# Performance work log

Hardware: AMD Instinct MI355X
Metric: run time of the kernel (lower is better)

Reference implementation:

```python
import jax, jax.numpy as jnp
import numpy as np

N_C, N_S, D = 16384, 16384, 2688  # 128x128 hypercolumn grid, VGG16 concat channels
EPS = 1e-8


def setup_inputs() -> dict:
    key = jax.random.key(0)
    k1, k2 = jax.random.split(key)
    feats_c = jax.random.normal(k1, (N_C, D), dtype=jnp.float32)
    feats_s = jax.random.normal(k2, (N_S, D), dtype=jnp.float32)
    return {"feats_c": feats_c, "feats_s": feats_s}


def reference(feats_c, feats_s):
    # NNST replace_features: for each content hypercolumn vector, find the
    # style feature vector with max cosine similarity and take it as target.
    cn = feats_c * jax.lax.rsqrt(jnp.sum(feats_c * feats_c, axis=1, keepdims=True) + EPS)
    sn = feats_s * jax.lax.rsqrt(jnp.sum(feats_s * feats_s, axis=1, keepdims=True) + EPS)
    sim = jnp.einsum("cd,sd->cs", cn, sn)  # [N_C, N_S] cosine similarity
    idx = jnp.argmax(sim, axis=1)           # nearest style feature per content pixel
    target_feats = jnp.take(feats_s, idx, axis=0)  # gather un-normalized style feats
    return target_feats
```

## Files before the change

### kernel.cpp

```cpp
#include <hip/hip_runtime.h>
#include <stdint.h>

typedef unsigned short ushort_t;
typedef unsigned int u32;
typedef unsigned long long u64;

#define NC_ 16384
#define NS_ 16384
#define DIM 2688
#define D4 (DIM / 4)
#define KSTEPS (DIM / 32)

typedef __attribute__((ext_vector_type(8))) short short8;
typedef __attribute__((ext_vector_type(4))) float f32x4;


__device__ inline ushort_t f2bf(float x) {
  u32 u = __float_as_uint(x);
  u32 r = u + 0x7FFFu + ((u >> 16) & 1u);
  return (ushort_t)(r >> 16);
}
__device__ inline float bf2f(ushort_t b) { return __uint_as_float(((u32)b) << 16); }

__device__ inline u32 fkey(float f) {
  u32 u = __float_as_uint(f);
  return (u & 0x80000000u) ? ~u : (u | 0x80000000u);
}

__device__ inline void async16(const void* g, void* l) {
  __builtin_amdgcn_global_load_lds(
      (const __attribute__((address_space(1))) u32*)g,
      (__attribute__((address_space(3))) u32*)l, 16, 0, 0);
}


__global__ __launch_bounds__(256) void content_split_kernel(
    const float* __restrict__ fc, ushort_t* __restrict__ c_hi, ushort_t* __restrict__ c_lo) {
  size_t i = (size_t)blockIdx.x * 256 + threadIdx.x;
  if (i >= (size_t)NC_ * DIM / 4) return;
  float4 v = ((const float4*)fc)[i];
  ushort4 h, l;
  h.x = f2bf(v.x); l.x = f2bf(v.x - bf2f(h.x));
  h.y = f2bf(v.y); l.y = f2bf(v.y - bf2f(h.y));
  h.z = f2bf(v.z); l.z = f2bf(v.z - bf2f(h.z));
  h.w = f2bf(v.w); l.w = f2bf(v.w - bf2f(h.w));
  ((ushort4*)c_hi)[i] = h;
  ((ushort4*)c_lo)[i] = l;
}


__global__ __launch_bounds__(256) void style_split_kernel(
    const float* __restrict__ fs, ushort_t* __restrict__ s_hi, ushort_t* __restrict__ s_lo) {
  const int s = blockIdx.x, t = threadIdx.x;
  const float4* row = (const float4*)(fs + (size_t)s * DIM);
  float ss = 0.f;
  for (int i = t; i < D4; i += 256) {
    float4 v = row[i];
    ss += v.x * v.x + v.y * v.y + v.z * v.z + v.w * v.w;
  }
#pragma unroll
  for (int off = 32; off >= 1; off >>= 1) ss += __shfl_xor(ss, off, 64);
  __shared__ float wsum[4];
  if ((t & 63) == 0) wsum[t >> 6] = ss;
  __syncthreads();
  float scale = rsqrtf(wsum[0] + wsum[1] + wsum[2] + wsum[3] + 1e-8f);
  ushort4* h4 = (ushort4*)(s_hi + (size_t)s * DIM);
  ushort4* l4 = (ushort4*)(s_lo + (size_t)s * DIM);
  for (int i = t; i < D4; i += 256) {
    float4 v = row[i];
    float x = v.x * scale, y = v.y * scale, z = v.z * scale, w = v.w * scale;
    ushort4 h, l;
    h.x = f2bf(x); l.x = f2bf(x - bf2f(h.x));
    h.y = f2bf(y); l.y = f2bf(y - bf2f(h.y));
    h.z = f2bf(z); l.z = f2bf(z - bf2f(h.z));
    h.w = f2bf(w); l.w = f2bf(w - bf2f(h.w));
    h4[i] = h;
    l4[i] = l;
  }
}


__global__ __launch_bounds__(256) void sim_argmax_kernel(
    const ushort_t* __restrict__ c_hi, const ushort_t* __restrict__ c_lo,
    const ushort_t* __restrict__ s_hi, const ushort_t* __restrict__ s_lo,
    u64* __restrict__ partial) {
  __shared__ __align__(16) ushort_t lds[4 * 128 * 32];
  __shared__ u64 red[256];

  ushort_t* la_hi = lds;
  ushort_t* la_lo = lds + 4096;
  ushort_t* lb_hi = lds + 8192;
  ushort_t* lb_lo = lds + 12288;

  const int t = threadIdx.x;
  const int bid = blockIdx.x;
  const int grp = bid >> 8;
  const int wi = bid & 255;
  const int cb = (grp & 7) * 16 + (wi & 15);
  const int sb = (grp >> 3) * 16 + (wi >> 4);

  const ushort_t* gah = c_hi + (size_t)cb * 128 * DIM;
  const ushort_t* gal = c_lo + (size_t)cb * 128 * DIM;
  const ushort_t* gbh = s_hi + (size_t)sb * 128 * DIM;
  const ushort_t* gbl = s_lo + (size_t)sb * 128 * DIM;

  const int lane = t & 63;
  const int wave = t >> 6;
  const int wy = wave >> 1, wx = wave & 1;
  const int lm = lane & 15, q = lane >> 4;

  f32x4 acc[4][4];
#pragma unroll
  for (int i = 0; i < 4; i++)
#pragma unroll
    for (int j = 0; j < 4; j++) acc[i][j] = (f32x4){0.f, 0.f, 0.f, 0.f};

  const int tw = t & 192;

  for (int ks = 0; ks < KSTEPS; ++ks) {
    const int kel = ks * 32;
#pragma unroll
    for (int j = 0; j < 2; ++j) {
      int e = j * 256 + t;
      int row = e >> 2, c4 = e & 3;
      size_t goff = (size_t)row * DIM + kel + c4 * 8;
      int loff = (j * 256 + tw) * 8;
      async16(gah + goff, la_hi + loff);
      async16(gal + goff, la_lo + loff);
      async16(gbh + goff, lb_hi + loff);
      async16(gbl + goff, lb_lo + loff);
    }
    __syncthreads();

    short8 ah[4], al[4], bh[4], bl[4];
#pragma unroll
    for (int mi = 0; mi < 4; ++mi) {
      int r = (wy * 64 + mi * 16 + lm) * 32 + q * 8;
      ah[mi] = *(const short8*)(la_hi + r);
      al[mi] = *(const short8*)(la_lo + r);
    }
#pragma unroll
    for (int ni = 0; ni < 4; ++ni) {
      int r = (wx * 64 + ni * 16 + lm) * 32 + q * 8;
      bh[ni] = *(const short8*)(lb_hi + r);
      bl[ni] = *(const short8*)(lb_lo + r);
    }
#pragma unroll
    for (int mi = 0; mi < 4; ++mi)
#pragma unroll
      for (int ni = 0; ni < 4; ++ni) {
        acc[mi][ni] = __builtin_amdgcn_mfma_f32_16x16x32_bf16(ah[mi], bh[ni], acc[mi][ni], 0, 0, 0);
        acc[mi][ni] = __builtin_amdgcn_mfma_f32_16x16x32_bf16(ah[mi], bl[ni], acc[mi][ni], 0, 0, 0);
        acc[mi][ni] = __builtin_amdgcn_mfma_f32_16x16x32_bf16(al[mi], bh[ni], acc[mi][ni], 0, 0, 0);
      }
    __syncthreads();
  }

#pragma unroll
  for (int mi = 0; mi < 4; ++mi) {
#pragma unroll
    for (int r = 0; r < 4; ++r) {
      float bv = acc[mi][0][r];
      int bn = 0;
#pragma unroll
      for (int ni = 1; ni < 4; ++ni) {
        float v = acc[mi][ni][r];
        if (v > bv) { bv = v; bn = ni; }
      }
      u32 colg = (u32)(sb * 128 + wx * 64 + bn * 16 + lm);
      u64 key = ((u64)fkey(bv) << 32) | (u64)(0xFFFFFFFFu - colg);
#pragma unroll
      for (int off = 8; off >= 1; off >>= 1) {
        u64 o = __shfl_xor((unsigned long long)key, off, 64);
        if (o > key) key = o;
      }
      if (lm == 0) red[(wy * 64 + mi * 16 + q * 4 + r) * 2 + wx] = key;
    }
  }
  __syncthreads();
  if (t < 128) {
    u64 k0 = red[t * 2], k1 = red[t * 2 + 1];
    u64 b = k0 > k1 ? k0 : k1;
    partial[((size_t)(cb * 128 + t)) * 128 + sb] = b;
  }
}


__global__ __launch_bounds__(256) void argmax_gather_kernel(
    const u64* __restrict__ partial, const float* __restrict__ fs, float* __restrict__ out) {
  const int m = blockIdx.x, t = threadIdx.x;
  __shared__ u64 sred[2];
  u64 key = 0;
  if (t < 128) key = partial[(size_t)m * 128 + t];
#pragma unroll
  for (int off = 32; off >= 1; off >>= 1) {
    u64 o = __shfl_xor((unsigned long long)key, off, 64);
    if (o > key) key = o;
  }
  if (t < 128 && (t & 63) == 0) sred[t >> 6] = key;
  __syncthreads();
  u64 best = sred[0] > sred[1] ? sred[0] : sred[1];
  u32 col = 0xFFFFFFFFu - (u32)best;
  const float4* src = (const float4*)(fs + (size_t)col * DIM);
  float4* dst = (float4*)(out + (size_t)m * DIM);
  for (int i = t; i < D4; i += 256) dst[i] = src[i];
}


extern "C" void kernel_launch(void* const* d_in, const int* in_sizes, int n_in,
                              void* d_out, int out_size, void* d_ws, size_t ws_size,
                              hipStream_t stream) {
  const float* fc = (const float*)d_in[0];
  const float* fs = (const float*)d_in[1];
  float* out = (float*)d_out;

  ushort_t* c_hi = (ushort_t*)d_ws;
  ushort_t* c_lo = c_hi + (size_t)NC_ * DIM;
  ushort_t* s_hi = c_lo + (size_t)NC_ * DIM;
  ushort_t* s_lo = s_hi + (size_t)NS_ * DIM;
  u64* partial = (u64*)(s_lo + (size_t)NS_ * DIM);

  content_split_kernel<<<(NC_ * DIM / 4 + 255) / 256, 256, 0, stream>>>(fc, c_hi, c_lo);
  style_split_kernel<<<NS_, 256, 0, stream>>>(fs, s_hi, s_lo);
  sim_argmax_kernel<<<16384, 256, 0, stream>>>(c_hi, c_lo, s_hi, s_lo, partial);
  argmax_gather_kernel<<<NC_, 256, 0, stream>>>(partial, fs, out);
}
```

Baseline: 4.686 ms.

## Widen similarity tile to 128x256 and XOR-swizzle LDS layout

```diff
diff --git a/kernel.cpp b/kernel.cpp
--- a/kernel.cpp
+++ b/kernel.cpp
@@ -31,6 +31,10 @@
   __builtin_amdgcn_global_load_lds(
       (const __attribute__((address_space(1))) u32*)g,
       (__attribute__((address_space(3))) u32*)l, 16, 0, 0);
+}
+
+__device__ inline int swz(int r, int q) {
+  return ((r >> 1) << 6) + (((((r & 1) << 2) | q) ^ ((r >> 1) & 7)) << 3);
 }
 
 
@@ -80,17 +84,17 @@
 }
 
 
-__global__ __launch_bounds__(256) void sim_argmax_kernel(
+__global__ __launch_bounds__(256, 2) void sim_argmax_kernel(
     const ushort_t* __restrict__ c_hi, const ushort_t* __restrict__ c_lo,
     const ushort_t* __restrict__ s_hi, const ushort_t* __restrict__ s_lo,
     u64* __restrict__ partial) {
-  __shared__ __align__(16) ushort_t lds[4 * 128 * 32];
-  __shared__ u64 red[256];
+  __shared__ __align__(16) ushort_t lds[24576];
+  __shared__ u64 red[128][2];
 
   ushort_t* la_hi = lds;
   ushort_t* la_lo = lds + 4096;
   ushort_t* lb_hi = lds + 8192;
-  ushort_t* lb_lo = lds + 12288;
+  ushort_t* lb_lo = lds + 16384;
 
   const int t = threadIdx.x;
   const int bid = blockIdx.x;
@@ -101,19 +105,19 @@
 
   const ushort_t* gah = c_hi + (size_t)cb * 128 * DIM;
   const ushort_t* gal = c_lo + (size_t)cb * 128 * DIM;
-  const ushort_t* gbh = s_hi + (size_t)sb * 128 * DIM;
-  const ushort_t* gbl = s_lo + (size_t)sb * 128 * DIM;
+  const ushort_t* gbh = s_hi + (size_t)sb * 256 * DIM;
+  const ushort_t* gbl = s_lo + (size_t)sb * 256 * DIM;
 
   const int lane = t & 63;
   const int wave = t >> 6;
   const int wy = wave >> 1, wx = wave & 1;
   const int lm = lane & 15, q = lane >> 4;
 
-  f32x4 acc[4][4];
+  f32x4 acc[4][8];
 #pragma unroll
   for (int i = 0; i < 4; i++)
 #pragma unroll
-    for (int j = 0; j < 4; j++) acc[i][j] = (f32x4){0.f, 0.f, 0.f, 0.f};
+    for (int j = 0; j < 8; j++) acc[i][j] = (f32x4){0.f, 0.f, 0.f, 0.f};
 
   const int tw = t & 192;
 
@@ -122,37 +126,53 @@
 #pragma unroll
     for (int j = 0; j < 2; ++j) {
       int e = j * 256 + t;
-      int row = e >> 2, c4 = e & 3;
-      size_t goff = (size_t)row * DIM + kel + c4 * 8;
+      int rp = e >> 3;
+      int cc = (e & 7) ^ (rp & 7);
+      int row = (rp << 1) | (cc >> 2);
+      size_t goff = (size_t)row * DIM + kel + (cc & 3) * 8;
       int loff = (j * 256 + tw) * 8;
       async16(gah + goff, la_hi + loff);
       async16(gal + goff, la_lo + loff);
+    }
+#pragma unroll
+    for (int j = 0; j < 4; ++j) {
+      int e = j * 256 + t;
+      int rp = e >> 3;
+      int cc = (e & 7) ^ (rp & 7);
+      int row = (rp << 1) | (cc >> 2);
+      size_t goff = (size_t)row * DIM + kel + (cc & 3) * 8;
+      int loff = (j * 256 + tw) * 8;
       async16(gbh + goff, lb_hi + loff);
       async16(gbl + goff, lb_lo + loff);
     }
     __syncthreads();
 
-    short8 ah[4], al[4], bh[4], bl[4];
+    short8 ah[4], al[4];
 #pragma unroll
     for (int mi = 0; mi < 4; ++mi) {
-      int r = (wy * 64 + mi * 16 + lm) * 32 + q * 8;
+      int r = swz(wy * 64 + mi * 16 + lm, q);
       ah[mi] = *(const short8*)(la_hi + r);
       al[mi] = *(const short8*)(la_lo + r);
     }
 #pragma unroll
-    for (int ni = 0; ni < 4; ++ni) {
-      int r = (wx * 64 + ni * 16 + lm) * 32 + q * 8;
-      bh[ni] = *(const short8*)(lb_hi + r);
-      bl[ni] = *(const short8*)(lb_lo + r);
-    }
-#pragma unroll
-    for (int mi = 0; mi < 4; ++mi)
-#pragma unroll
-      for (int ni = 0; ni < 4; ++ni) {
-        acc[mi][ni] = __builtin_amdgcn_mfma_f32_16x16x32_bf16(ah[mi], bh[ni], acc[mi][ni], 0, 0, 0);
-        acc[mi][ni] = __builtin_amdgcn_mfma_f32_16x16x32_bf16(ah[mi], bl[ni], acc[mi][ni], 0, 0, 0);
-        acc[mi][ni] = __builtin_amdgcn_mfma_f32_16x16x32_bf16(al[mi], bh[ni], acc[mi][ni], 0, 0, 0);
+    for (int h = 0; h < 2; ++h) {
+      short8 bh[4], bl[4];
+#pragma unroll
+      for (int nj = 0; nj < 4; ++nj) {
+        int r = swz(wx * 128 + (h * 4 + nj) * 16 + lm, q);
+        bh[nj] = *(const short8*)(lb_hi + r);
+        bl[nj] = *(const short8*)(lb_lo + r);
       }
+#pragma unroll
+      for (int mi = 0; mi < 4; ++mi)
+#pragma unroll
+        for (int nj = 0; nj < 4; ++nj) {
+          int ni = h * 4 + nj;
+          acc[mi][ni] = __builtin_amdgcn_mfma_f32_16x16x32_bf16(ah[mi], bh[nj], acc[mi][ni], 0, 0, 0);
+          acc[mi][ni] = __builtin_amdgcn_mfma_f32_16x16x32_bf16(ah[mi], bl[nj], acc[mi][ni], 0, 0, 0);
+          acc[mi][ni] = __builtin_amdgcn_mfma_f32_16x16x32_bf16(al[mi], bh[nj], acc[mi][ni], 0, 0, 0);
+        }
+    }
     __syncthreads();
   }
 
@@ -163,25 +183,25 @@
       float bv = acc[mi][0][r];
       int bn = 0;
 #pragma unroll
-      for (int ni = 1; ni < 4; ++ni) {
+      for (int ni = 1; ni < 8; ++ni) {
         float v = acc[mi][ni][r];
         if (v > bv) { bv = v; bn = ni; }
       }
-      u32 colg = (u32)(sb * 128 + wx * 64 + bn * 16 + lm);
+      u32 colg = (u32)(sb * 256 + wx * 128 + bn * 16 + lm);
       u64 key = ((u64)fkey(bv) << 32) | (u64)(0xFFFFFFFFu - colg);
 #pragma unroll
       for (int off = 8; off >= 1; off >>= 1) {
         u64 o = __shfl_xor((unsigned long long)key, off, 64);
         if (o > key) key = o;
       }
-      if (lm == 0) red[(wy * 64 + mi * 16 + q * 4 + r) * 2 + wx] = key;
+      if (lm == 0) red[wy * 64 + mi * 16 + q * 4 + r][wx] = key;
     }
   }
   __syncthreads();
   if (t < 128) {
-    u64 k0 = red[t * 2], k1 = red[t * 2 + 1];
+    u64 k0 = red[t][0], k1 = red[t][1];
     u64 b = k0 > k1 ? k0 : k1;
-    partial[((size_t)(cb * 128 + t)) * 128 + sb] = b;
+    partial[((size_t)(cb * 128 + t)) * 64 + sb] = b;
   }
 }
 
@@ -189,17 +209,18 @@
 __global__ __launch_bounds__(256) void argmax_gather_kernel(
     const u64* __restrict__ partial, const float* __restrict__ fs, float* __restrict__ out) {
   const int m = blockIdx.x, t = threadIdx.x;
-  __shared__ u64 sred[2];
-  u64 key = 0;
-  if (t < 128) key = partial[(size_t)m * 128 + t];
-#pragma unroll
-  for (int off = 32; off >= 1; off >>= 1) {
-    u64 o = __shfl_xor((unsigned long long)key, off, 64);
-    if (o > key) key = o;
-  }
-  if (t < 128 && (t & 63) == 0) sred[t >> 6] = key;
+  __shared__ u64 sbest;
+  if (t < 64) {
+    u64 key = partial[(size_t)m * 64 + t];
+#pragma unroll
+    for (int off = 32; off >= 1; off >>= 1) {
+      u64 o = __shfl_xor((unsigned long long)key, off, 64);
+      if (o > key) key = o;
+    }
+    if (t == 0) sbest = key;
+  }
   __syncthreads();
-  u64 best = sred[0] > sred[1] ? sred[0] : sred[1];
+  u64 best = sbest;
   u32 col = 0xFFFFFFFFu - (u32)best;
   const float4* src = (const float4*)(fs + (size_t)col * DIM);
   float4* dst = (float4*)(out + (size_t)m * DIM);
@@ -222,6 +243,6 @@
 
   content_split_kernel<<<(NC_ * DIM / 4 + 255) / 256, 256, 0, stream>>>(fc, c_hi, c_lo);
   style_split_kernel<<<NS_, 256, 0, stream>>>(fs, s_hi, s_lo);
-  sim_argmax_kernel<<<16384, 256, 0, stream>>>(c_hi, c_lo, s_hi, s_lo, partial);
+  sim_argmax_kernel<<<8192, 256, 0, stream>>>(c_hi, c_lo, s_hi, s_lo, partial);
   argmax_gather_kernel<<<NC_, 256, 0, stream>>>(partial, fs, out);
 }
```

Result: faster. 3.815 ms (-18.6%).
